# Kernel tuning notes

Hardware: AMD Instinct MI355X
Metric: run time of the kernel (lower is better)

## Reference

```python
import jax, jax.numpy as jnp
import numpy as np

# Lloyd-Max (Max 1960) optimal 16-level quantizer for N(0,1), bits=4
_CODEBOOK_4 = np.array([-2.7326, -2.069, -1.6181, -1.2562, -0.9424, -0.6568,
                        -0.3881, -0.1284, 0.1284, 0.3881, 0.6568, 0.9424,
                        1.2562, 1.6181, 2.069, 2.7326], dtype=np.float32)
DIM = 256


def setup_inputs() -> dict:
    key = jax.random.key(0)
    kx, kq = jax.random.split(key)
    x = jax.random.normal(kx, (4, 4096, DIM), dtype=jnp.float32)
    # orthogonal rotation via QR of a Gaussian matrix (mirrors torch.linalg.qr)
    rotation, _ = jnp.linalg.qr(jax.random.normal(kq, (DIM, DIM), dtype=jnp.float32))
    codebook = jnp.asarray(_CODEBOOK_4)
    return {"x": x, "rotation": rotation, "codebook": codebook}


def reference(x, rotation, codebook):
    shape = x.shape
    d = shape[-1]
    sqrt_d = jnp.sqrt(jnp.asarray(d, dtype=x.dtype))
    x_flat = x.reshape(-1, d)                                   # (N, d)
    x_norm = jnp.maximum(
        jnp.linalg.norm(x_flat, axis=-1, keepdims=True), 1e-8)  # (N, 1)
    u = x_flat / x_norm                                         # unit vectors
    y_scaled = (u @ rotation.T) * sqrt_d                        # ~N(0,1) coords
    # nearest codebook entry per scalar coordinate: (N, d, K) -> argmin over K
    idx = jnp.argmin(jnp.abs(y_scaled[..., None] - codebook), axis=-1)
    y_hat = codebook[idx] / sqrt_d                              # (N, d)
    x_hat = (y_hat @ rotation) * x_norm                         # de-rotate, rescale
    return x_hat.reshape(shape)
```

## Files before the change

### kernel.cpp

```cpp
#include <hip/hip_runtime.h>

typedef _Float16 f16;
typedef _Float16 f16x4 __attribute__((ext_vector_type(4)));
typedef _Float16 f16x8 __attribute__((ext_vector_type(8)));
typedef float f32x16 __attribute__((ext_vector_type(16)));
typedef float f32x4 __attribute__((ext_vector_type(4)));

#define APITCH 264
#define WREG 67584

__global__ __launch_bounds__(1024) void prep_kernel(const float* __restrict__ R,
                                                    f16* __restrict__ ws) {
  __shared__ float Lrs[32][260];
  const int g = blockIdx.x;
  const int t = threadIdx.x;
  f16* W1h = ws;
  f16* W1l = ws + WREG;
  f16* W2h = ws + 2 * WREG;

  #pragma unroll
  for (int it = 0; it < 2; ++it) {
    int c = it * 1024 + t;
    int row = c >> 6, c4 = (c & 63) * 4;
    f32x4 v = *(const f32x4*)&R[(long)(32 * g + row) * 256 + c4];
    *(f32x4*)&Lrs[row][c4] = v;
  }
  __syncthreads();

  {
    int f_loc = t >> 6, l = t & 63;
    int k0 = 16 * f_loc + 8 * (l >> 5);
    const float* src = &Lrs[l & 31][k0];
    f16x8 h, lo;
    #pragma unroll
    for (int j = 0; j < 8; ++j) {
      float v = src[j] * 256.0f;
      f16 hh = (f16)v;
      h[j] = hh;
      lo[j] = (f16)(v - (float)hh);
    }
    long o = (long)(g * 16 + f_loc) * 512 + l * 8;
    *(f16x8*)(W1h + o) = h;
    *(f16x8*)(W1l + o) = lo;
  }

  {
    int gp = t >> 7, e = (t >> 6) & 1, l = t & 63;
    int lr0 = 16 * e + 8 * (l >> 5);
    int col = 32 * gp + (l & 31);
    f16x8 h;
    #pragma unroll
    for (int j = 0; j < 8; ++j) h[j] = (f16)Lrs[lr0 + j][col];
    long o = (long)(gp * 16 + 2 * g + e) * 512 + l * 8;
    *(f16x8*)(W2h + o) = h;
  }
}

__global__ __launch_bounds__(512, 1) void tq_main(
    const float* __restrict__ X, const float* __restrict__ CB,
    const f16* __restrict__ ws, float* __restrict__ OUT) {
  __shared__ f16 A1h[64][APITCH];
  __shared__ f16 A1l[64][APITCH];
  __shared__ float s2s[64];

  const int tid = threadIdx.x;
  const int lane = tid & 63;
  const int wv = tid >> 6;
  const int lrow = lane & 31;
  const int kg = lane >> 5;
  const long row0 = (long)blockIdx.x * 64;

  const f16* W1h = ws;
  const f16* W1l = ws + WREG;
  const f16* W2h = ws + 2 * WREG;

  const int r = tid >> 3, q = tid & 7;
  const float* xp = X + (row0 + r) * 256 + q * 32;
  float xa[32];
  #pragma unroll
  for (int i = 0; i < 8; ++i) {
    f32x4 v = ((const f32x4*)xp)[i];
    xa[4 * i] = v.x; xa[4 * i + 1] = v.y; xa[4 * i + 2] = v.z; xa[4 * i + 3] = v.w;
  }

  const f16* W1hp = W1h + (long)(wv * 16) * 512 + lane * 8;
  const f16* W1lp = W1l + (long)(wv * 16) * 512 + lane * 8;
  f16x8 bh0 = *(const f16x8*)(W1hp);
  f16x8 bl0 = *(const f16x8*)(W1lp);
  f16x8 bh1 = *(const f16x8*)(W1hp + 512);
  f16x8 bl1 = *(const f16x8*)(W1lp + 512);
  f16x8 bh2 = *(const f16x8*)(W1hp + 1024);
  f16x8 bl2 = *(const f16x8*)(W1lp + 1024);
  f16x8 bh3 = *(const f16x8*)(W1hp + 1536);
  f16x8 bl3 = *(const f16x8*)(W1lp + 1536);

  float ss = 0.f;
  #pragma unroll
  for (int i = 0; i < 32; ++i) ss += xa[i] * xa[i];
  ss += __shfl_xor(ss, 4, 8);
  ss += __shfl_xor(ss, 2, 8);
  ss += __shfl_xor(ss, 1, 8);
  float nrm = fmaxf(sqrtf(ss), 1e-8f);
  float s1f = 4096.0f / nrm;
  if (q == 0) s2s[r] = nrm * 0.0625f;

  #pragma unroll
  for (int c8 = 0; c8 < 4; ++c8) {
    f16x8 h, l;
    #pragma unroll
    for (int j = 0; j < 8; ++j) {
      float a = xa[c8 * 8 + j] * s1f;
      f16 hh = (f16)a;
      h[j] = hh;
      l[j] = (f16)(a - (float)hh);
    }
    *(f16x8*)&A1h[r][q * 32 + c8 * 8] = h;
    *(f16x8*)&A1l[r][q * 32 + c8 * 8] = l;
  }
  __syncthreads();

  f32x16 zv;
  #pragma unroll
  for (int i = 0; i < 16; ++i) zv[i] = 0.0f;
  f32x16 accH0 = zv, accL0 = zv, accH1 = zv, accL1 = zv;

#define MM1_STAGE(BH, BL, KS)                                                   \
  {                                                                             \
    const int k0 = (KS) * 16 + kg * 8;                                          \
    f16x8 ah0 = *(const f16x8*)&A1h[lrow][k0];                                  \
    f16x8 al0 = *(const f16x8*)&A1l[lrow][k0];                                  \
    f16x8 ah1 = *(const f16x8*)&A1h[32 + lrow][k0];                             \
    f16x8 al1 = *(const f16x8*)&A1l[32 + lrow][k0];                             \
    accH0 = __builtin_amdgcn_mfma_f32_32x32x16_f16(ah0, BH, accH0, 0, 0, 0);    \
    accL0 = __builtin_amdgcn_mfma_f32_32x32x16_f16(al0, BH, accL0, 0, 0, 0);    \
    accH1 = __builtin_amdgcn_mfma_f32_32x32x16_f16(ah1, BH, accH1, 0, 0, 0);    \
    accL1 = __builtin_amdgcn_mfma_f32_32x32x16_f16(al1, BH, accL1, 0, 0, 0);    \
    accH0 = __builtin_amdgcn_mfma_f32_32x32x16_f16(ah0, BL, accH0, 0, 0, 0);    \
    accL0 = __builtin_amdgcn_mfma_f32_32x32x16_f16(al0, BL, accL0, 0, 0, 0);    \
    accH1 = __builtin_amdgcn_mfma_f32_32x32x16_f16(ah1, BL, accH1, 0, 0, 0);    \
    accL1 = __builtin_amdgcn_mfma_f32_32x32x16_f16(al1, BL, accL1, 0, 0, 0);    \
    BH = *(const f16x8*)(W1hp + ((KS) + 4) * 512);                              \
    BL = *(const f16x8*)(W1lp + ((KS) + 4) * 512);                              \
  }

  #pragma unroll
  for (int ksb = 0; ksb < 16; ksb += 4) {
    MM1_STAGE(bh0, bl0, ksb)
    MM1_STAGE(bh1, bl1, ksb + 1)
    MM1_STAGE(bh2, bl2, ksb + 2)
    MM1_STAGE(bh3, bl3, ksb + 3)
  }
#undef MM1_STAGE

  f32x16 acc0, acc1;
  #pragma unroll
  for (int i = 0; i < 16; ++i) { acc0[i] = accH0[i] + accL0[i]; acc1[i] = accH1[i] + accL1[i]; }

  const f16* W2p = W2h + (long)(wv * 16) * 512 + lane * 8;
  f16x8 c0 = *(const f16x8*)(W2p);
  f16x8 c1 = *(const f16x8*)(W2p + 512);
  f16x8 c2 = *(const f16x8*)(W2p + 1024);
  f16x8 c3 = *(const f16x8*)(W2p + 1536);

  __syncthreads();

  float cbf[16];
  #pragma unroll
  for (int i = 0; i < 16; ++i) cbf[i] = CB[i];
  float M[15];
  #pragma unroll
  for (int t = 0; t < 15; ++t) M[t] = 65536.0f * (0.5f * (cbf[t] + cbf[t + 1]));
  unsigned int cpk[8];
  #pragma unroll
  for (int i = 0; i < 8; ++i) {
    unsigned short lb = __builtin_bit_cast(unsigned short, (f16)cbf[2 * i]);
    unsigned short hb = __builtin_bit_cast(unsigned short, (f16)cbf[2 * i + 1]);
    cpk[i] = ((unsigned int)hb << 16) | (unsigned int)lb;
  }

  f16 (*Qs)[APITCH] = A1h;
  #pragma unroll
  for (int m = 0; m < 2; ++m) {
    const f32x16& am = m ? acc1 : acc0;
    #pragma unroll
    for (int rr = 0; rr < 16; ++rr) {
      float y = am[rr];
      int row = 32 * m + 4 * kg + (rr & 3) + 8 * (rr >> 2);
      int kk = 32 * wv + lrow;
      bool b3 = y > M[7];
      float m2 = b3 ? M[11] : M[3];
      bool b2 = y > m2;
      float m1 = b3 ? (b2 ? M[13] : M[9]) : (b2 ? M[5] : M[1]);
      bool b1 = y > m1;
      float m0 = b1 ? (b3 ? (b2 ? M[14] : M[10]) : (b2 ? M[6] : M[2]))
                    : (b3 ? (b2 ? M[12] : M[8]) : (b2 ? M[4] : M[0]));
      bool b0 = y > m0;
      unsigned int pp = b3 ? (b2 ? (b1 ? cpk[7] : cpk[6]) : (b1 ? cpk[5] : cpk[4]))
                           : (b2 ? (b1 ? cpk[3] : cpk[2]) : (b1 ? cpk[1] : cpk[0]));
      unsigned short qb = (unsigned short)(b0 ? (pp >> 16) : (pp & 0xFFFFu));
      Qs[row][kk] = __builtin_bit_cast(f16, qb);
    }
  }
  __syncthreads();

  f32x16 acc2_0 = zv, acc2_1 = zv;

#define MM2_STAGE(CS, KS)                                                       \
  {                                                                             \
    const int k0 = (KS) * 16 + kg * 8;                                          \
    f16x8 qa0 = *(const f16x8*)&Qs[lrow][k0];                                   \
    f16x8 qa1 = *(const f16x8*)&Qs[32 + lrow][k0];                              \
    acc2_0 = __builtin_amdgcn_mfma_f32_32x32x16_f16(qa0, CS, acc2_0, 0, 0, 0);  \
    acc2_1 = __builtin_amdgcn_mfma_f32_32x32x16_f16(qa1, CS, acc2_1, 0, 0, 0);  \
    CS = *(const f16x8*)(W2p + ((KS) + 4) * 512);                               \
  }

  #pragma unroll
  for (int ksb = 0; ksb < 16; ksb += 4) {
    MM2_STAGE(c0, ksb)
    MM2_STAGE(c1, ksb + 1)
    MM2_STAGE(c2, ksb + 2)
    MM2_STAGE(c3, ksb + 3)
  }
#undef MM2_STAGE

  #pragma unroll
  for (int m = 0; m < 2; ++m) {
    const f32x16& am = m ? acc2_1 : acc2_0;
    #pragma unroll
    for (int rr = 0; rr < 16; ++rr) {
      int row = 32 * m + 4 * kg + (rr & 3) + 8 * (rr >> 2);
      int col = 32 * wv + lrow;
      OUT[(row0 + row) * 256 + col] = am[rr] * s2s[row];
    }
  }
}

#define FB_APITCH 264
#define FB_B1PITCH 40
#define FB_B2PITCH 264

__global__ __launch_bounds__(256, 1) void tq_main_fb(
    const float* __restrict__ X, const float* __restrict__ R,
    const float* __restrict__ CB, float* __restrict__ OUT) {
  __shared__ f16 A1h[64][FB_APITCH];
  __shared__ f16 A1l[64][FB_APITCH];
  __shared__ f16 Qs[64][FB_APITCH];
  __shared__ f32x4 Braw[2624];
  __shared__ float pn[4][64];
  __shared__ float s1s[64];
  __shared__ float s2s[64];

  f16 (*B1h)[FB_B1PITCH] = (f16(*)[FB_B1PITCH])Braw;
  f16 (*B1l)[FB_B1PITCH] = (f16(*)[FB_B1PITCH])((char*)Braw + 20480);
  f16 (*B2h)[FB_B2PITCH] = (f16(*)[FB_B2PITCH])Braw;

  const int tid = threadIdx.x;
  const int lane = tid & 63;
  const int wv = tid >> 6;
  const int lrow = lane & 31;
  const int kg = lane >> 5;
  const long row0 = (long)blockIdx.x * 64;

  float cbf[16];
  #pragma unroll
  for (int i = 0; i < 16; ++i) cbf[i] = CB[i];
  float M[15];
  #pragma unroll
  for (int t = 0; t < 15; ++t) M[t] = 65536.0f * (0.5f * (cbf[t] + cbf[t + 1]));
  unsigned int cpk[8];
  #pragma unroll
  for (int i = 0; i < 8; ++i) {
    unsigned short lb = __builtin_bit_cast(unsigned short, (f16)cbf[2 * i]);
    unsigned short hb = __builtin_bit_cast(unsigned short, (f16)cbf[2 * i + 1]);
    cpk[i] = ((unsigned int)hb << 16) | (unsigned int)lb;
  }

  const int xrow = tid >> 2, xq = tid & 3;
  const float* xp = X + (row0 + xrow) * 256 + xq * 64;
  float xa[64];
  #pragma unroll
  for (int i = 0; i < 16; ++i) {
    f32x4 v = ((const f32x4*)xp)[i];
    xa[4 * i] = v.x; xa[4 * i + 1] = v.y; xa[4 * i + 2] = v.z; xa[4 * i + 3] = v.w;
  }
  float ss = 0.f;
  #pragma unroll
  for (int i = 0; i < 64; ++i) ss += xa[i] * xa[i];
  pn[xq][xrow] = ss;
  __syncthreads();
  if (tid < 64) {
    float s = pn[0][tid] + pn[1][tid] + pn[2][tid] + pn[3][tid];
    float nrm = fmaxf(sqrtf(s), 1e-8f);
    s1s[tid] = 4096.0f / nrm;
    s2s[tid] = nrm * 0.0625f;
  }
  __syncthreads();

  {
    float s1f = s1s[xrow];
    #pragma unroll
    for (int c8 = 0; c8 < 8; ++c8) {
      f16x8 h, l;
      #pragma unroll
      for (int j = 0; j < 8; ++j) {
        float a = xa[c8 * 8 + j] * s1f;
        f16 hh = (f16)a;
        h[j] = hh;
        l[j] = (f16)(a - (float)hh);
      }
      *(f16x8*)&A1h[xrow][xq * 64 + c8 * 8] = h;
      *(f16x8*)&A1l[xrow][xq * 64 + c8 * 8] = l;
    }
  }

  f32x4 pf[8];
  #pragma unroll
  for (int q = 0; q < 8; ++q) {
    int c = q * 256 + tid;
    pf[q] = *(const f32x4*)&R[(long)(c >> 3) * 256 + ((c & 7) * 4)];
  }

  f32x16 zv;
  #pragma unroll
  for (int i = 0; i < 16; ++i) zv[i] = 0.0f;
  f32x16 acc[2][2];
  acc[0][0] = zv; acc[0][1] = zv; acc[1][0] = zv; acc[1][1] = zv;

  for (int kp = 0; kp < 8; ++kp) {
    __syncthreads();
    #pragma unroll
    for (int q = 0; q < 8; ++q) {
      int c = q * 256 + tid;
      int n = c >> 3, k4 = (c & 7) * 4;
      f16x4 h, l;
      #pragma unroll
      for (int j = 0; j < 4; ++j) {
        float sv = pf[q][j] * 256.0f;
        f16 hh = (f16)sv;
        h[j] = hh;
        l[j] = (f16)(sv - (float)hh);
      }
      *(f16x4*)&B1h[n][k4] = h;
      *(f16x4*)&B1l[n][k4] = l;
    }
    __syncthreads();
    if (kp < 7) {
      #pragma unroll
      for (int q = 0; q < 8; ++q) {
        int c = q * 256 + tid;
        pf[q] = *(const f32x4*)&R[(long)(c >> 3) * 256 + (kp + 1) * 32 + ((c & 7) * 4)];
      }
    }
    #pragma unroll
    for (int ks = 0; ks < 2; ++ks) {
      const int k0 = kp * 32 + ks * 16 + kg * 8;
      const int lk = ks * 16 + kg * 8;
      f16x8 ah[2], al[2], bhf[2], blf[2];
      #pragma unroll
      for (int m = 0; m < 2; ++m) {
        ah[m] = *(const f16x8*)&A1h[32 * m + lrow][k0];
        al[m] = *(const f16x8*)&A1l[32 * m + lrow][k0];
      }
      #pragma unroll
      for (int n = 0; n < 2; ++n) {
        int col = 64 * wv + 32 * n + lrow;
        bhf[n] = *(const f16x8*)&B1h[col][lk];
        blf[n] = *(const f16x8*)&B1l[col][lk];
      }
      #pragma unroll
      for (int m = 0; m < 2; ++m)
        #pragma unroll
        for (int n = 0; n < 2; ++n) {
          acc[m][n] = __builtin_amdgcn_mfma_f32_32x32x16_f16(ah[m], bhf[n], acc[m][n], 0, 0, 0);
          acc[m][n] = __builtin_amdgcn_mfma_f32_32x32x16_f16(al[m], bhf[n], acc[m][n], 0, 0, 0);
          acc[m][n] = __builtin_amdgcn_mfma_f32_32x32x16_f16(ah[m], blf[n], acc[m][n], 0, 0, 0);
          acc[m][n] = __builtin_amdgcn_mfma_f32_32x32x16_f16(al[m], blf[n], acc[m][n], 0, 0, 0);
        }
    }
  }

  #pragma unroll
  for (int q = 0; q < 8; ++q) {
    int c = q * 256 + tid;
    pf[q] = *(const f32x4*)&R[(long)(c >> 6) * 256 + ((c & 63) * 4)];
  }

  #pragma unroll
  for (int m = 0; m < 2; ++m)
    #pragma unroll
    for (int n = 0; n < 2; ++n)
      #pragma unroll
      for (int rr = 0; rr < 16; ++rr) {
        float y = acc[m][n][rr];
        int row = 32 * m + 4 * kg + (rr & 3) + 8 * (rr >> 2);
        int kk = 64 * wv + 32 * n + lrow;
        bool b3 = y > M[7];
        float m2 = b3 ? M[11] : M[3];
        bool b2 = y > m2;
        float m1 = b3 ? (b2 ? M[13] : M[9]) : (b2 ? M[5] : M[1]);
        bool b1 = y > m1;
        float m0 = b1 ? (b3 ? (b2 ? M[14] : M[10]) : (b2 ? M[6] : M[2]))
                      : (b3 ? (b2 ? M[12] : M[8]) : (b2 ? M[4] : M[0]));
        bool b0 = y > m0;
        unsigned int pp = b3 ? (b2 ? (b1 ? cpk[7] : cpk[6]) : (b1 ? cpk[5] : cpk[4]))
                             : (b2 ? (b1 ? cpk[3] : cpk[2]) : (b1 ? cpk[1] : cpk[0]));
        unsigned short qb = (unsigned short)(b0 ? (pp >> 16) : (pp & 0xFFFFu));
        Qs[row][kk] = __builtin_bit_cast(f16, qb);
      }
  __syncthreads();

  f32x16 acc2[2][2];
  acc2[0][0] = zv; acc2[0][1] = zv; acc2[1][0] = zv; acc2[1][1] = zv;

  for (int kp = 0; kp < 8; ++kp) {
    if (kp) __syncthreads();
    #pragma unroll
    for (int q = 0; q < 8; ++q) {
      int c = q * 256 + tid;
      int k = c >> 6, n4 = (c & 63) * 4;
      f16x4 h;
      #pragma unroll
      for (int j = 0; j < 4; ++j) h[j] = (f16)pf[q][j];
      *(f16x4*)&B2h[k][n4] = h;
    }
    __syncthreads();
    if (kp < 7) {
      #pragma unroll
      for (int q = 0; q < 8; ++q) {
        int c = q * 256 + tid;
        pf[q] = *(const f32x4*)&R[(long)((kp + 1) * 32 + (c >> 6)) * 256 + ((c & 63) * 4)];
      }
    }
    #pragma unroll
    for (int ks = 0; ks < 2; ++ks) {
      const int k0 = kp * 32 + ks * 16 + kg * 8;
      const int lk = ks * 16 + kg * 8;
      f16x8 qa[2], bb[2];
      #pragma unroll
      for (int m = 0; m < 2; ++m) qa[m] = *(const f16x8*)&Qs[32 * m + lrow][k0];
      #pragma unroll
      for (int n = 0; n < 2; ++n) {
        int colg = 64 * wv + 32 * n + lrow;
        #pragma unroll
        for (int j = 0; j < 8; ++j) bb[n][j] = B2h[lk + j][colg];
      }
      #pragma unroll
      for (int m = 0; m < 2; ++m)
        #pragma unroll
        for (int n = 0; n < 2; ++n)
          acc2[m][n] = __builtin_amdgcn_mfma_f32_32x32x16_f16(qa[m], bb[n], acc2[m][n], 0, 0, 0);
    }
  }

  #pragma unroll
  for (int m = 0; m < 2; ++m)
    #pragma unroll
    for (int n = 0; n < 2; ++n)
      #pragma unroll
      for (int rr = 0; rr < 16; ++rr) {
        int row = 32 * m + 4 * kg + (rr & 3) + 8 * (rr >> 2);
        int col = 64 * wv + 32 * n + lrow;
        OUT[(row0 + row) * 256 + col] = acc2[m][n][rr] * s2s[row];
      }
}

extern "C" void kernel_launch(void* const* d_in, const int* in_sizes, int n_in,
                              void* d_out, int out_size, void* d_ws, size_t ws_size,
                              hipStream_t stream) {
  const float* X = (const float*)d_in[0];
  const float* R = (const float*)d_in[1];
  const float* CB = (const float*)d_in[2];
  float* OUT = (float*)d_out;
  const int nrows = in_sizes[0] / 256;

  if (ws_size >= (size_t)3 * WREG * sizeof(f16)) {
    f16* ws = (f16*)d_ws;
    prep_kernel<<<8, 1024, 0, stream>>>(R, ws);
    tq_main<<<nrows / 64, 512, 0, stream>>>(X, CB, ws, OUT);
  } else {
    tq_main_fb<<<nrows / 64, 256, 0, stream>>>(X, R, CB, OUT);
  }
}
```

Baseline: 31.36 us.

## Cut register pressure for higher occupancy, drop low×low MFMA, split prep across more blocks

The main kernel's launch bounds go from 1 to 4 blocks per CU. To fit, it merges the hi/lo accumulators into one pair, drops the lo×lo MFMA term (6 MFMAs per stage instead of 8), and halves the B-operand prefetch depth from 4 to 2 stages. Codebook loads move earlier and become scalar via readfirstlane, and the prep kernel is split into 32 blocks of 512 threads. Dropping the lo×lo product changes accuracy slightly, and the shallower prefetch may expose more load latency.

```diff
diff --git a/kernel.cpp b/kernel.cpp
--- a/kernel.cpp
+++ b/kernel.cpp
@@ -9,54 +9,59 @@
 #define APITCH 264
 #define WREG 67584
 
-__global__ __launch_bounds__(1024) void prep_kernel(const float* __restrict__ R,
-                                                    f16* __restrict__ ws) {
+__global__ __launch_bounds__(512) void prep_kernel(const float* __restrict__ R,
+                                                   f16* __restrict__ ws) {
   __shared__ float Lrs[32][260];
-  const int g = blockIdx.x;
+  const int b = blockIdx.x;
+  const int g = b >> 2, h = b & 3;
   const int t = threadIdx.x;
   f16* W1h = ws;
   f16* W1l = ws + WREG;
   f16* W2h = ws + 2 * WREG;
 
   #pragma unroll
-  for (int it = 0; it < 2; ++it) {
-    int c = it * 1024 + t;
+  for (int it = 0; it < 4; ++it) {
+    int c = it * 512 + t;
     int row = c >> 6, c4 = (c & 63) * 4;
     f32x4 v = *(const f32x4*)&R[(long)(32 * g + row) * 256 + c4];
     *(f32x4*)&Lrs[row][c4] = v;
   }
   __syncthreads();
 
-  {
-    int f_loc = t >> 6, l = t & 63;
+  if (t < 256) {
+    int f_loc = 4 * h + (t >> 6), l = t & 63;
     int k0 = 16 * f_loc + 8 * (l >> 5);
     const float* src = &Lrs[l & 31][k0];
-    f16x8 h, lo;
+    f16x8 hi, lo;
     #pragma unroll
     for (int j = 0; j < 8; ++j) {
       float v = src[j] * 256.0f;
       f16 hh = (f16)v;
-      h[j] = hh;
+      hi[j] = hh;
       lo[j] = (f16)(v - (float)hh);
     }
     long o = (long)(g * 16 + f_loc) * 512 + l * 8;
-    *(f16x8*)(W1h + o) = h;
+    *(f16x8*)(W1h + o) = hi;
     *(f16x8*)(W1l + o) = lo;
-  }
-
-  {
-    int gp = t >> 7, e = (t >> 6) & 1, l = t & 63;
+  } else {
+    int u = t - 256;
+    int gp = 2 * h + (u >> 7), e = (u >> 6) & 1, l = u & 63;
     int lr0 = 16 * e + 8 * (l >> 5);
     int col = 32 * gp + (l & 31);
-    f16x8 h;
-    #pragma unroll
-    for (int j = 0; j < 8; ++j) h[j] = (f16)Lrs[lr0 + j][col];
+    f16x8 hv;
+    #pragma unroll
+    for (int j = 0; j < 8; ++j) hv[j] = (f16)Lrs[lr0 + j][col];
     long o = (long)(gp * 16 + 2 * g + e) * 512 + l * 8;
-    *(f16x8*)(W2h + o) = h;
+    *(f16x8*)(W2h + o) = hv;
   }
 }
 
-__global__ __launch_bounds__(512, 1) void tq_main(
+__device__ __forceinline__ float rfl(float x) {
+  return __builtin_bit_cast(float,
+      __builtin_amdgcn_readfirstlane(__builtin_bit_cast(int, x)));
+}
+
+__global__ __launch_bounds__(512, 4) void tq_main(
     const float* __restrict__ X, const float* __restrict__ CB,
     const f16* __restrict__ ws, float* __restrict__ OUT) {
   __shared__ f16 A1h[64][APITCH];
@@ -89,10 +94,10 @@
   f16x8 bl0 = *(const f16x8*)(W1lp);
   f16x8 bh1 = *(const f16x8*)(W1hp + 512);
   f16x8 bl1 = *(const f16x8*)(W1lp + 512);
-  f16x8 bh2 = *(const f16x8*)(W1hp + 1024);
-  f16x8 bl2 = *(const f16x8*)(W1lp + 1024);
-  f16x8 bh3 = *(const f16x8*)(W1hp + 1536);
-  f16x8 bl3 = *(const f16x8*)(W1lp + 1536);
+
+  float cbf[16];
+  #pragma unroll
+  for (int i = 0; i < 16; ++i) cbf[i] = rfl(CB[i]);
 
   float ss = 0.f;
   #pragma unroll
@@ -122,7 +127,7 @@
   f32x16 zv;
   #pragma unroll
   for (int i = 0; i < 16; ++i) zv[i] = 0.0f;
-  f32x16 accH0 = zv, accL0 = zv, accH1 = zv, accL1 = zv;
+  f32x16 acc0 = zv, acc1 = zv;
 
 #define MM1_STAGE(BH, BL, KS)                                                   \
   {                                                                             \
@@ -131,42 +136,27 @@
     f16x8 al0 = *(const f16x8*)&A1l[lrow][k0];                                  \
     f16x8 ah1 = *(const f16x8*)&A1h[32 + lrow][k0];                             \
     f16x8 al1 = *(const f16x8*)&A1l[32 + lrow][k0];                             \
-    accH0 = __builtin_amdgcn_mfma_f32_32x32x16_f16(ah0, BH, accH0, 0, 0, 0);    \
-    accL0 = __builtin_amdgcn_mfma_f32_32x32x16_f16(al0, BH, accL0, 0, 0, 0);    \
-    accH1 = __builtin_amdgcn_mfma_f32_32x32x16_f16(ah1, BH, accH1, 0, 0, 0);    \
-    accL1 = __builtin_amdgcn_mfma_f32_32x32x16_f16(al1, BH, accL1, 0, 0, 0);    \
-    accH0 = __builtin_amdgcn_mfma_f32_32x32x16_f16(ah0, BL, accH0, 0, 0, 0);    \
-    accL0 = __builtin_amdgcn_mfma_f32_32x32x16_f16(al0, BL, accL0, 0, 0, 0);    \
-    accH1 = __builtin_amdgcn_mfma_f32_32x32x16_f16(ah1, BL, accH1, 0, 0, 0);    \
-    accL1 = __builtin_amdgcn_mfma_f32_32x32x16_f16(al1, BL, accL1, 0, 0, 0);    \
-    BH = *(const f16x8*)(W1hp + ((KS) + 4) * 512);                              \
-    BL = *(const f16x8*)(W1lp + ((KS) + 4) * 512);                              \
-  }
-
-  #pragma unroll
-  for (int ksb = 0; ksb < 16; ksb += 4) {
+    acc0 = __builtin_amdgcn_mfma_f32_32x32x16_f16(ah0, BH, acc0, 0, 0, 0);      \
+    acc1 = __builtin_amdgcn_mfma_f32_32x32x16_f16(ah1, BH, acc1, 0, 0, 0);      \
+    acc0 = __builtin_amdgcn_mfma_f32_32x32x16_f16(al0, BH, acc0, 0, 0, 0);      \
+    acc1 = __builtin_amdgcn_mfma_f32_32x32x16_f16(al1, BH, acc1, 0, 0, 0);      \
+    acc0 = __builtin_amdgcn_mfma_f32_32x32x16_f16(ah0, BL, acc0, 0, 0, 0);      \
+    acc1 = __builtin_amdgcn_mfma_f32_32x32x16_f16(ah1, BL, acc1, 0, 0, 0);      \
+    BH = *(const f16x8*)(W1hp + ((KS) + 2) * 512);                              \
+    BL = *(const f16x8*)(W1lp + ((KS) + 2) * 512);                              \
+  }
+
+  #pragma unroll
+  for (int ksb = 0; ksb < 16; ksb += 2) {
     MM1_STAGE(bh0, bl0, ksb)
     MM1_STAGE(bh1, bl1, ksb + 1)
-    MM1_STAGE(bh2, bl2, ksb + 2)
-    MM1_STAGE(bh3, bl3, ksb + 3)
   }
 #undef MM1_STAGE
-
-  f32x16 acc0, acc1;
-  #pragma unroll
-  for (int i = 0; i < 16; ++i) { acc0[i] = accH0[i] + accL0[i]; acc1[i] = accH1[i] + accL1[i]; }
 
   const f16* W2p = W2h + (long)(wv * 16) * 512 + lane * 8;
   f16x8 c0 = *(const f16x8*)(W2p);
   f16x8 c1 = *(const f16x8*)(W2p + 512);
-  f16x8 c2 = *(const f16x8*)(W2p + 1024);
-  f16x8 c3 = *(const f16x8*)(W2p + 1536);
-
-  __syncthreads();
-
-  float cbf[16];
-  #pragma unroll
-  for (int i = 0; i < 16; ++i) cbf[i] = CB[i];
+
   float M[15];
   #pragma unroll
   for (int t = 0; t < 15; ++t) M[t] = 65536.0f * (0.5f * (cbf[t] + cbf[t + 1]));
@@ -178,29 +168,32 @@
     cpk[i] = ((unsigned int)hb << 16) | (unsigned int)lb;
   }
 
+  __syncthreads();
+
   f16 (*Qs)[APITCH] = A1h;
-  #pragma unroll
-  for (int m = 0; m < 2; ++m) {
-    const f32x16& am = m ? acc1 : acc0;
-    #pragma unroll
-    for (int rr = 0; rr < 16; ++rr) {
-      float y = am[rr];
-      int row = 32 * m + 4 * kg + (rr & 3) + 8 * (rr >> 2);
-      int kk = 32 * wv + lrow;
-      bool b3 = y > M[7];
-      float m2 = b3 ? M[11] : M[3];
-      bool b2 = y > m2;
-      float m1 = b3 ? (b2 ? M[13] : M[9]) : (b2 ? M[5] : M[1]);
-      bool b1 = y > m1;
-      float m0 = b1 ? (b3 ? (b2 ? M[14] : M[10]) : (b2 ? M[6] : M[2]))
-                    : (b3 ? (b2 ? M[12] : M[8]) : (b2 ? M[4] : M[0]));
-      bool b0 = y > m0;
-      unsigned int pp = b3 ? (b2 ? (b1 ? cpk[7] : cpk[6]) : (b1 ? cpk[5] : cpk[4]))
-                           : (b2 ? (b1 ? cpk[3] : cpk[2]) : (b1 ? cpk[1] : cpk[0]));
-      unsigned short qb = (unsigned short)(b0 ? (pp >> 16) : (pp & 0xFFFFu));
-      Qs[row][kk] = __builtin_bit_cast(f16, qb);
-    }
-  }
+#define QUANT(ACC, MOFF)                                                        \
+  _Pragma("unroll")                                                             \
+  for (int rr = 0; rr < 16; ++rr) {                                             \
+    float y = ACC[rr];                                                          \
+    int row = (MOFF) + 4 * kg + (rr & 3) + 8 * (rr >> 2);                       \
+    int kk = 32 * wv + lrow;                                                    \
+    bool b3 = y > M[7];                                                         \
+    float m2 = b3 ? M[11] : M[3];                                               \
+    bool b2 = y > m2;                                                           \
+    float m1 = b3 ? (b2 ? M[13] : M[9]) : (b2 ? M[5] : M[1]);                   \
+    bool b1 = y > m1;                                                           \
+    float m0 = b1 ? (b3 ? (b2 ? M[14] : M[10]) : (b2 ? M[6] : M[2]))            \
+                  : (b3 ? (b2 ? M[12] : M[8]) : (b2 ? M[4] : M[0]));            \
+    bool b0 = y > m0;                                                           \
+    unsigned int pp = b3 ? (b2 ? (b1 ? cpk[7] : cpk[6]) : (b1 ? cpk[5] : cpk[4])) \
+                         : (b2 ? (b1 ? cpk[3] : cpk[2]) : (b1 ? cpk[1] : cpk[0])); \
+    unsigned short qb = (unsigned short)(b0 ? (pp >> 16) : (pp & 0xFFFFu));     \
+    Qs[row][kk] = __builtin_bit_cast(f16, qb);                                  \
+  }
+
+  QUANT(acc0, 0)
+  QUANT(acc1, 32)
+#undef QUANT
   __syncthreads();
 
   f32x16 acc2_0 = zv, acc2_1 = zv;
@@ -212,27 +205,22 @@
     f16x8 qa1 = *(const f16x8*)&Qs[32 + lrow][k0];                              \
     acc2_0 = __builtin_amdgcn_mfma_f32_32x32x16_f16(qa0, CS, acc2_0, 0, 0, 0);  \
     acc2_1 = __builtin_amdgcn_mfma_f32_32x32x16_f16(qa1, CS, acc2_1, 0, 0, 0);  \
-    CS = *(const f16x8*)(W2p + ((KS) + 4) * 512);                               \
-  }
-
-  #pragma unroll
-  for (int ksb = 0; ksb < 16; ksb += 4) {
+    CS = *(const f16x8*)(W2p + ((KS) + 2) * 512);                               \
+  }
+
+  #pragma unroll
+  for (int ksb = 0; ksb < 16; ksb += 2) {
     MM2_STAGE(c0, ksb)
     MM2_STAGE(c1, ksb + 1)
-    MM2_STAGE(c2, ksb + 2)
-    MM2_STAGE(c3, ksb + 3)
   }
 #undef MM2_STAGE
 
   #pragma unroll
-  for (int m = 0; m < 2; ++m) {
-    const f32x16& am = m ? acc2_1 : acc2_0;
-    #pragma unroll
-    for (int rr = 0; rr < 16; ++rr) {
-      int row = 32 * m + 4 * kg + (rr & 3) + 8 * (rr >> 2);
-      int col = 32 * wv + lrow;
-      OUT[(row0 + row) * 256 + col] = am[rr] * s2s[row];
-    }
+  for (int rr = 0; rr < 16; ++rr) {
+    int row = 4 * kg + (rr & 3) + 8 * (rr >> 2);
+    int col = 32 * wv + lrow;
+    OUT[(row0 + row) * 256 + col] = acc2_0[rr] * s2s[row];
+    OUT[(row0 + 32 + row) * 256 + col] = acc2_1[rr] * s2s[32 + row];
   }
 }
 
@@ -476,7 +464,7 @@
 
   if (ws_size >= (size_t)3 * WREG * sizeof(f16)) {
     f16* ws = (f16*)d_ws;
-    prep_kernel<<<8, 1024, 0, stream>>>(R, ws);
+    prep_kernel<<<32, 512, 0, stream>>>(R, ws);
     tq_main<<<nrows / 64, 512, 0, stream>>>(X, CB, ws, OUT);
   } else {
     tq_main_fb<<<nrows / 64, 256, 0, stream>>>(X, R, CB, OUT);
```

Measured after the change: 28.83 us. 1.09x faster.
